# Kernel tuning notes

Hardware: AMD Instinct MI355X
Metric: run time of the kernel (lower is better)

Reference implementation:

```python
import jax, jax.numpy as jnp
import numpy as np

BN_EPS = 1e-5


def _tconv(X, w1, b1, w2, b2, w3, b3):
    # X: (B, T, N, C) -> conv over time with kernel (1, k), gated GLU-style
    Xp = X.transpose(0, 2, 1, 3)  # (B, N, T, C)
    def conv(w, b):
        return jax.lax.conv_general_dilated(
            Xp, w, (1, 1), 'VALID',
            dimension_numbers=('NHWC', 'HWIO', 'NHWC')) + b
    P = conv(w1, b1)
    Q = jax.nn.sigmoid(conv(w2, b2))
    R = conv(w3, b3)
    H = jax.nn.relu(P * Q + R)
    return H.transpose(0, 2, 1, 3)  # (B, T-k+1, N, Cout)


def _cheb(x, ei, W, b):
    # Batched ChebConv (sym norm, lambda_max=2 => L_hat = -D^-1/2 A D^-1/2)
    # x: (S, N, F), ei: (S, 2, E), W: (K, F, Fout)
    S, N, F = x.shape
    row, col = ei[:, 0], ei[:, 1]           # (S, E)
    ones = jnp.ones(ei.shape[-1], x.dtype)
    def norm_one(r, c):
        deg = jax.ops.segment_sum(ones, r, num_segments=N)
        dis = jnp.where(deg > 0, jax.lax.rsqrt(jnp.maximum(deg, 1.)), 0.)
        return -dis[r] * dis[c]
    w = jax.vmap(norm_one)(row, col)        # (S, E), constant wrt floats
    def prop(xs, r, c, ws):
        return jax.ops.segment_sum(ws[:, None] * xs[c], r, num_segments=N)
    propv = jax.vmap(prop)
    Tx = [x, propv(x, row, col, w)]
    for _ in range(W.shape[0] - 2):
        Tx.append(2. * propv(Tx[-1], row, col, w) - Tx[-2])
    return jnp.einsum('ksnf,kfo->sno', jnp.stack(Tx), W) + b


def _forward(X, tc1_w1, tc1_b1, tc1_w2, tc1_b2, tc1_w3, tc1_b3,
             cheb_w, cheb_b,
             tc2_w1, tc2_b1, tc2_w2, tc2_b2, tc2_w3, tc2_b3,
             bn_gamma, bn_beta, conv3_w, conv3_b, f1_w, f1_b, edge_index):
    T0 = _tconv(X, tc1_w1, tc1_b1, tc1_w2, tc1_b2, tc1_w3, tc1_b3)  # (B,38,N,H)
    B, Tt, N, H = T0.shape
    ei = edge_index[:, :Tt].reshape(B * Tt, 2, edge_index.shape[-1])
    G = _cheb(T0.reshape(B * Tt, N, H), ei, cheb_w, cheb_b)
    G = jax.nn.relu(G.reshape(B, Tt, N, H))
    T2 = _tconv(G, tc2_w1, tc2_b1, tc2_w2, tc2_b2, tc2_w3, tc2_b3)  # (B,36,N,Co)
    # BatchNorm2d over channel dim = num_nodes (training-mode batch stats)
    Tn = T2.transpose(0, 2, 1, 3)  # (B, N, T, C)
    mean = Tn.mean(axis=(0, 2, 3), keepdims=True)
    var = Tn.var(axis=(0, 2, 3), keepdims=True)
    Tn = (Tn - mean) * jax.lax.rsqrt(var + BN_EPS)
    Tn = Tn * bn_gamma[None, :, None, None] + bn_beta[None, :, None, None]
    Tb = Tn.transpose(0, 2, 1, 3)                 # (B, T, N, C)
    Tr = Tb.reshape(B, Tb.shape[1], -1)           # (B, T, N*C=3200)
    y = jax.lax.conv_general_dilated(
        Tr[:, None, :, :], conv3_w, (1, 1), 'VALID',
        dimension_numbers=('NCHW', 'OIHW', 'NCHW'))  # (B,128,T-2,1)
    y = y + conv3_b[None, :, None, None]
    y = y[:, :, :, 0]
    pooled = y.mean(axis=2)                        # AvgPool1d over full length
    return pooled @ f1_w + f1_b                    # (B, 3200)


def setup_inputs() -> dict:
    key = jax.random.key(0)
    ks = jax.random.split(key, 20)
    B, Tw, N, Cin, H, Co, E = 32, 40, 50, 2, 128, 64, 800
    KT, K = 3, 3
    s = 0.05
    d = {
        'X': jax.random.normal(ks[0], (B, Tw, N, Cin), jnp.float32),
        'edge_index': jax.random.randint(ks[1], (B, Tw, 2, E), 0, N),
        'tc1_w1': jax.random.normal(ks[2], (1, KT, Cin, H), jnp.float32) * s,
        'tc1_b1': jnp.zeros((H,), jnp.float32),
        'tc1_w2': jax.random.normal(ks[3], (1, KT, Cin, H), jnp.float32) * s,
        'tc1_b2': jnp.zeros((H,), jnp.float32),
        'tc1_w3': jax.random.normal(ks[4], (1, KT, Cin, H), jnp.float32) * s,
        'tc1_b3': jnp.zeros((H,), jnp.float32),
        'cheb_w': jax.random.normal(ks[5], (K, H, H), jnp.float32) * s,
        'cheb_b': jnp.zeros((H,), jnp.float32),
        'tc2_w1': jax.random.normal(ks[6], (1, KT, H, Co), jnp.float32) * s,
        'tc2_b1': jnp.zeros((Co,), jnp.float32),
        'tc2_w2': jax.random.normal(ks[7], (1, KT, H, Co), jnp.float32) * s,
        'tc2_b2': jnp.zeros((Co,), jnp.float32),
        'tc2_w3': jax.random.normal(ks[8], (1, KT, H, Co), jnp.float32) * s,
        'tc2_b3': jnp.zeros((Co,), jnp.float32),
        'bn_gamma': jnp.ones((N,), jnp.float32),
        'bn_beta': jnp.zeros((N,), jnp.float32),
        'conv3_w': jax.random.normal(ks[9], (128, 1, 3, N * Co), jnp.float32) * 0.01,
        'conv3_b': jnp.zeros((128,), jnp.float32),
        'f1_w': jax.random.normal(ks[10], (128, N * Co), jnp.float32) * s,
        'f1_b': jnp.zeros((N * Co,), jnp.float32),
    }
    return d


def reference(X, tc1_w1, tc1_b1, tc1_w2, tc1_b2, tc1_w3, tc1_b3,
              cheb_w, cheb_b,
              tc2_w1, tc2_b1, tc2_w2, tc2_b2, tc2_w3, tc2_b3,
              bn_gamma, bn_beta, conv3_w, conv3_b, f1_w, f1_b, edge_index):
    return _forward(X, tc1_w1, tc1_b1, tc1_w2, tc1_b2, tc1_w3, tc1_b3,
                    cheb_w, cheb_b,
                    tc2_w1, tc2_b1, tc2_w2, tc2_b2, tc2_w3, tc2_b3,
                    bn_gamma, bn_beta, conv3_w, conv3_b, f1_w, f1_b, edge_index)
```

## Files before the change

kernel.cpp:

```cpp
#include <hip/hip_runtime.h>
#include <hip/hip_bf16.h>

#define BB 32
#define TW 40
#define NN 50
#define HH 128
#define CO 64
#define EE 800
#define TT 38
#define TT2 36
#define TPOOL 34
#define NCO 3200
#define SS (BB*TT)
#define NPAD 64
#define RPAD (SS*NPAD)

#define PB_US ((size_t)RPAD * HH)
#define PB_BYTES (PB_US * 2)

typedef __attribute__((ext_vector_type(8))) short s16x8;
typedef __attribute__((ext_vector_type(16))) float f32x16;
typedef unsigned short us;

static __device__ __forceinline__ unsigned int f2bf_u(float x) {
    unsigned int u = __float_as_uint(x);
    return (u + 0x7fffu + ((u >> 16) & 1u)) >> 16;
}
static __device__ __forceinline__ float bfu2f(unsigned int h) {
    return __uint_as_float(h << 16);
}
static __device__ __forceinline__ size_t fragoff32(int m, int c) {
    return (size_t)(c >> 4) * 512 + ((c >> 3) & 1) * 256 + m * 8 + (c & 7);
}
#define MFMA(a, b, c) __builtin_amdgcn_mfma_f32_32x32x16_bf16((a), (b), (c), 0, 0, 0)

__global__ __launch_bounds__(256) void k_wprep(
    const float* __restrict__ cw,
    const float* __restrict__ tw1, const float* __restrict__ tw2, const float* __restrict__ tw3,
    us* __restrict__ VTh, us* __restrict__ VTl,
    us* __restrict__ WTh,
    float* __restrict__ pooled)
{
    int idx = blockIdx.x * 256 + threadIdx.x;
    float v; int col, k; bool wantlo;
    us *dh, *dl;
    if (idx < 128 * 384) {
        col = idx / 384; k = idx % 384;
        if (k < 128)      v = cw[k * 128 + col] - cw[32768 + k * 128 + col];
        else if (k < 256) v = cw[16384 + (k - 128) * 128 + col];
        else              v = 2.f * cw[32768 + (k - 256) * 128 + col];
        dh = VTh; dl = VTl; wantlo = true;
    } else if (idx < 128 * 384 + 192 * 384) {
        int i2 = idx - 128 * 384;
        col = i2 / 384; k = i2 % 384;
        int gg = col >> 6, o = col & 63;
        const float* src = (gg == 0) ? tw1 : (gg == 1) ? tw2 : tw3;
        v = src[k * 64 + o];
        dh = WTh; dl = 0; wantlo = false;
    } else {
        int z = idx - (128 * 384 + 192 * 384);
        if (z < 4096) pooled[z] = 0.f;
        return;
    }
    size_t off = ((size_t)((col >> 5) * 24 + (k >> 4)) * 64 + ((k >> 3) & 1) * 32 + (col & 31)) * 8
               + (k & 7);
    unsigned int h = f2bf_u(v);
    dh[off] = (us)h;
    if (wantlo) dl[off] = (us)f2bf_u(v - bfu2f(h));
}

#define TAS 136
#define TBS 72
#define LMS 53
__global__ __launch_bounds__(256) void k_cheb(
    const int* __restrict__ EI, const float* __restrict__ X,
    const float* __restrict__ w1, const float* __restrict__ b1,
    const float* __restrict__ w2, const float* __restrict__ b2,
    const float* __restrict__ w3, const float* __restrict__ b3,
    const us* __restrict__ VTh, const us* __restrict__ VTl,
    const float* __restrict__ bias,
    us* __restrict__ Gh)
{
    __shared__ __align__(16) char smem[61440];
    us* TbA = (us*)smem;
    us* TbB = (us*)(smem + 17408);
    us* Pa  = (us*)(smem + 35840);
    float* Lm = (float*)(smem + 35840);
    us* LA  = (us*)(smem + 53248);
    float* Xs = (float*)(smem + 53248);
    int* deg  = (int*)(smem + 53248 + 1216);
    float* dis = (float*)(smem + 53248 + 1216 + 224);

    int g = blockIdx.x;
    int tid = threadIdx.x;
    int b = g / TT, t = g % TT;
    const int* row = EI + (size_t)(b * TW + t) * 2 * EE;
    const int* col = row + EE;

    {
        s16x8 zz = {0, 0, 0, 0, 0, 0, 0, 0};
        for (int i = tid; i < 2240; i += 256) ((s16x8*)smem)[i] = zz;
    }
    for (int i = tid; i < 52 * LMS; i += 256) Lm[i] = 0.f;
    for (int i = tid; i < 300; i += 256) Xs[i] = X[(size_t)(b * TW + t) * 100 + i];
    if (tid < NN) deg[tid] = 0;
    __syncthreads();

    {
        int c = tid & 127, nh = tid >> 7;
        float wr1[6], wr2[6], wr3[6];
#pragma unroll
        for (int q = 0; q < 6; q++) {
            wr1[q] = w1[q * HH + c];
            wr2[q] = w2[q * HH + c];
            wr3[q] = w3[q * HH + c];
        }
        float bv1 = b1[c], bv2 = b2[c], bv3 = b3[c];
        for (int n = nh; n < NN; n += 2) {
            float P = bv1, Q = bv2, R = bv3;
#pragma unroll
            for (int q = 0; q < 6; q++) {
                float x = Xs[(q >> 1) * 100 + n * 2 + (q & 1)];
                P += x * wr1[q]; Q += x * wr2[q]; R += x * wr3[q];
            }
            float sg = 1.f / (1.f + expf(-Q));
            float v = P * sg + R;
            v = v > 0.f ? v : 0.f;
            us h = (us)f2bf_u(v);
            TbA[n * TAS + c] = h;
            TbB[c * TBS + n] = h;
        }
    }
    __syncthreads();
    for (int e = tid; e < EE; e += 256) atomicAdd(&deg[row[e]], 1);
    __syncthreads();
    if (tid < NN) dis[tid] = deg[tid] > 0 ? rsqrtf((float)deg[tid]) : 0.f;
    __syncthreads();
    for (int e = tid; e < EE; e += 256) {
        int r = row[e], cc = col[e];
        atomicAdd(&Lm[r * LMS + cc], -dis[r] * dis[cc]);
    }
    __syncthreads();
    for (int ent = tid; ent < 512; ent += 256) {
        int lanee = ent & 63;
        int ks = (ent >> 6) & 3;
        int mt = ent >> 8;
        int m = mt * 32 + (lanee & 31);
        int kb = ks * 16 + (lanee >> 5) * 8;
        s16x8 v;
#pragma unroll
        for (int j = 0; j < 8; j++) {
            int k = kb + j;
            float lv = (m < NN && k < NN) ? Lm[m * LMS + k] : 0.f;
            v[j] = (short)f2bf_u(lv);
        }
        *(s16x8*)(LA + ent * 8) = v;
    }
    __syncthreads();

    int lane = tid & 63;
    int w = tid >> 6;
    int rg = w >> 1, fh = w & 1;
    int nl = lane & 31;
    int khalf = lane >> 5;
    size_t laneoff = (size_t)lane * 8;

    const us* vh0 = VTh + (size_t)(fh * 2) * 12288 + laneoff;
    const us* vh1 = VTh + (size_t)(fh * 2 + 1) * 12288 + laneoff;
    const us* vl0 = VTl + (size_t)(fh * 2) * 12288 + laneoff;
    const us* vl1 = VTl + (size_t)(fh * 2 + 1) * 12288 + laneoff;

    int mrowA = rg * 32 + nl;
    int kbb = khalf * 8;

    f32x16 gacc0, gacc1, d0, d1;
#pragma unroll
    for (int r = 0; r < 16; r++) { gacc0[r] = 0.f; gacc1[r] = 0.f; d0[r] = 0.f; d1[r] = 0.f; }

#pragma unroll
    for (int ks = 0; ks < 4; ks++) {
        s16x8 afr = *(const s16x8*)(LA + ((rg * 4 + ks) * 64 + lane) * 8);
        int kb = ks * 16 + kbb;
        s16x8 bf0 = *(const s16x8*)(TbB + (fh * 64 + nl) * TBS + kb);
        s16x8 bf1 = *(const s16x8*)(TbB + (fh * 64 + 32 + nl) * TBS + kb);
        d0 = MFMA(afr, bf0, d0);
        d1 = MFMA(afr, bf1, d1);
    }
#pragma unroll
    for (int ks = 0; ks < 8; ks++) {
        s16x8 ah = *(const s16x8*)(TbA + mrowA * TAS + ks * 16 + kbb);
        s16x8 bh0 = *(const s16x8*)(vh0 + ks * 512);
        s16x8 bl0 = *(const s16x8*)(vl0 + ks * 512);
        s16x8 bh1 = *(const s16x8*)(vh1 + ks * 512);
        s16x8 bl1 = *(const s16x8*)(vl1 + ks * 512);
        gacc0 = MFMA(ah, bh0, gacc0); gacc0 = MFMA(ah, bl0, gacc0);
        gacc1 = MFMA(ah, bh1, gacc1); gacc1 = MFMA(ah, bl1, gacc1);
    }
    __syncthreads();
#pragma unroll
    for (int r = 0; r < 16; r++) {
        int mrow = (r & 3) + 8 * (r >> 2) + 4 * khalf;
        int node = rg * 32 + mrow;
        int f0 = fh * 64 + nl, f1 = f0 + 32;
        us h0 = (us)f2bf_u(d0[r]);
        us h1 = (us)f2bf_u(d1[r]);
        Pa[node * TAS + f0] = h0;
        Pa[node * TAS + f1] = h1;
        TbB[f0 * TBS + node] = h0;
        TbB[f1 * TBS + node] = h1;
    }
    __syncthreads();

#pragma unroll
    for (int r = 0; r < 16; r++) { d0[r] = 0.f; d1[r] = 0.f; }
#pragma unroll
    for (int ks = 0; ks < 4; ks++) {
        s16x8 afr = *(const s16x8*)(LA + ((rg * 4 + ks) * 64 + lane) * 8);
        int kb = ks * 16 + kbb;
        s16x8 bf0 = *(const s16x8*)(TbB + (fh * 64 + nl) * TBS + kb);
        s16x8 bf1 = *(const s16x8*)(TbB + (fh * 64 + 32 + nl) * TBS + kb);
        d0 = MFMA(afr, bf0, d0);
        d1 = MFMA(afr, bf1, d1);
    }
#pragma unroll
    for (int ks = 0; ks < 8; ks++) {
        s16x8 ah = *(const s16x8*)(Pa + mrowA * TAS + ks * 16 + kbb);
        s16x8 bh0 = *(const s16x8*)(vh0 + (8 + ks) * 512);
        s16x8 bh1 = *(const s16x8*)(vh1 + (8 + ks) * 512);
        gacc0 = MFMA(ah, bh0, gacc0);
        gacc1 = MFMA(ah, bh1, gacc1);
    }
    __syncthreads();
#pragma unroll
    for (int r = 0; r < 16; r++) {
        int mrow = (r & 3) + 8 * (r >> 2) + 4 * khalf;
        int node = rg * 32 + mrow;
        int f0 = fh * 64 + nl, f1 = f0 + 32;
        Pa[node * TAS + f0] = (us)f2bf_u(d0[r]);
        Pa[node * TAS + f1] = (us)f2bf_u(d1[r]);
    }
    __syncthreads();
#pragma unroll
    for (int ks = 0; ks < 8; ks++) {
        s16x8 ah = *(const s16x8*)(Pa + mrowA * TAS + ks * 16 + kbb);
        s16x8 bh0 = *(const s16x8*)(vh0 + (16 + ks) * 512);
        s16x8 bh1 = *(const s16x8*)(vh1 + (16 + ks) * 512);
        gacc0 = MFMA(ah, bh0, gacc0);
        gacc1 = MFMA(ah, bh1, gacc1);
    }

    int c0 = fh * 64 + nl, c1 = c0 + 32;
    float bv0 = bias[c0], bv1 = bias[c1];
    size_t gb = (size_t)g * 8192 + (size_t)rg * 4096;
#pragma unroll
    for (int r = 0; r < 16; r++) {
        int mrow = (r & 3) + 8 * (r >> 2) + 4 * khalf;
        float v0 = gacc0[r] + bv0; v0 = v0 > 0.f ? v0 : 0.f;
        float v1 = gacc1[r] + bv1; v1 = v1 > 0.f ? v1 : 0.f;
        Gh[gb + fragoff32(mrow, c0)] = (us)f2bf_u(v0);
        Gh[gb + fragoff32(mrow, c1)] = (us)f2bf_u(v1);
    }
}

__global__ __launch_bounds__(128) void k_tc2(
    const us* __restrict__ Gh,
    const us* __restrict__ WTh,
    const float* __restrict__ tb1, const float* __restrict__ tb2, const float* __restrict__ tb3,
    us* __restrict__ T2)
{
    int tid = threadIdx.x;
    int lane = tid & 63;
    int w = tid >> 6;
    int nl = lane & 31;
    size_t laneoff = (size_t)lane * 8;
    int i = blockIdx.x;
    int vb = (i & 7) * 288 + (i >> 3);
    int bt36 = vb >> 1, ntile = vb & 1;
    int b = bt36 / TT2, t = bt36 % TT2;

    const us* A[3];
#pragma unroll
    for (int k3 = 0; k3 < 3; k3++)
        A[k3] = Gh + (size_t)(b * TT + t + k3) * 8192 + (size_t)ntile * 4096 + laneoff;
    const us* Bh[3];
#pragma unroll
    for (int g3 = 0; g3 < 3; g3++)
        Bh[g3] = WTh + (size_t)(g3 * 2 + w) * 12288 + laneoff;

    f32x16 aP, aQ, aR;
#pragma unroll
    for (int r = 0; r < 16; r++) { aP[r] = 0.f; aQ[r] = 0.f; aR[r] = 0.f; }

#pragma unroll
    for (int k3 = 0; k3 < 3; k3++) {
#pragma unroll
        for (int ls = 0; ls < 8; ls++) {
            int offB = (k3 * 8 + ls) * 512;
            s16x8 a0 = *(const s16x8*)(A[k3] + ls * 512);
            s16x8 ph = *(const s16x8*)(Bh[0] + offB);
            s16x8 qh = *(const s16x8*)(Bh[1] + offB);
            s16x8 rh = *(const s16x8*)(Bh[2] + offB);
            aP = MFMA(a0, ph, aP);
            aQ = MFMA(a0, qh, aQ);
            aR = MFMA(a0, rh, aR);
        }
    }

    int o = w * 32 + nl;
    float bP = tb1[o], bQ = tb2[o], bR = tb3[o];
    int rbase = (lane >> 5) * 4;
#pragma unroll
    for (int r = 0; r < 16; r++) {
        int m = (r & 3) + 8 * (r >> 2) + rbase;
        int node = ntile * 32 + m;
        if (node < NN) {
            float P = aP[r] + bP, Q = aQ[r] + bQ, R = aR[r] + bR;
            float sg = 1.f / (1.f + expf(-Q));
            float v = P * sg + R;
            v = v > 0.f ? v : 0.f;
            T2[((size_t)bt36 * NN + node) * CO + o] = (us)f2bf_u(v);
        }
    }
}

__global__ __launch_bounds__(256) void k_bnpart(const us* __restrict__ T2, float* __restrict__ partial)
{
    int n = blockIdx.x >> 3, c = blockIdx.x & 7;
    int tid = threadIdx.x;
    float s = 0.f, ss = 0.f;
    for (int i = tid; i < 144 * 64; i += 256) {
        int bt = c * 144 + (i >> 6), o = i & 63;
        float v = bfu2f(T2[((size_t)bt * NN + n) * CO + o]);
        s += v; ss += v * v;
    }
    for (int off = 32; off > 0; off >>= 1) { s += __shfl_down(s, off, 64); ss += __shfl_down(ss, off, 64); }
    __shared__ float rs[4], rss[4];
    int lane = tid & 63, wv = tid >> 6;
    if (lane == 0) { rs[wv] = s; rss[wv] = ss; }
    __syncthreads();
    if (tid == 0) {
        partial[n * 8 + c] = rs[0] + rs[1] + rs[2] + rs[3];
        partial[400 + n * 8 + c] = rss[0] + rss[1] + rss[2] + rss[3];
    }
}

__global__ __launch_bounds__(64) void k_bnfin(const float* __restrict__ partial, float* __restrict__ stats)
{
    int n = threadIdx.x;
    if (n < NN) {
        float s = 0.f, ss = 0.f;
#pragma unroll
        for (int c = 0; c < 8; c++) { s += partial[n * 8 + c]; ss += partial[400 + n * 8 + c]; }
        const float inv = 1.f / (float)(BB * TT2 * CO);
        float m = s * inv;
        float var = ss * inv - m * m;
        stats[n] = m;
        stats[64 + n] = rsqrtf(var + 1e-5f);
    }
}

__global__ __launch_bounds__(256) void k_upool(
    const us* __restrict__ T2, const float* __restrict__ stats,
    const float* __restrict__ gamma, const float* __restrict__ beta,
    const float* __restrict__ W3, float* __restrict__ pooled)
{
    __shared__ __align__(16) float Ul[48 * 36 + 32];
    __shared__ float Ws[128 * 9];
    int blk = blockIdx.x;
    int jc = blk * 16;
    int n0 = jc >> 6;
    int tid = threadIdx.x;
    float mn = stats[n0], is = stats[64 + n0];
    float sc = is * gamma[n0];
    float off = (float)TPOOL * beta[n0] - (float)TPOOL * mn * sc;

    {
        int j = tid & 15, b0 = tid >> 4;
#pragma unroll
        for (int bp = 0; bp < 2; bp++) {
            int bb = b0 + 16 * bp;
            const us* p = T2 + (size_t)bb * TT2 * NCO + jc + j;
            float s0 = 0.f;
            for (int t = 0; t < TPOOL; t++) s0 += bfu2f(p[(size_t)t * NCO]);
            float s1 = s0 - bfu2f(p[0]) + bfu2f(p[(size_t)34 * NCO]);
            float s2 = s1 - bfu2f(p[(size_t)1 * NCO]) + bfu2f(p[(size_t)35 * NCO]);
            Ul[(0 * 16 + j) * 36 + bb] = s0 * sc + off;
            Ul[(1 * 16 + j) * 36 + bb] = s1 * sc + off;
            Ul[(2 * 16 + j) * 36 + bb] = s2 * sc + off;
        }
    }
    __syncthreads();

    int o = tid & 127, bq = tid >> 7;
    float acc[16];
#pragma unroll
    for (int i = 0; i < 16; i++) acc[i] = 0.f;

    for (int kjc = 0; kjc < 48; kjc += 8) {
        __syncthreads();
#pragma unroll
        for (int p4 = 0; p4 < 4; p4++) {
            int idx = p4 * 256 + tid;
            int oo = idx >> 3, q = idx & 7;
            int kj = kjc + q;
            Ws[oo * 9 + q] = W3[(size_t)oo * 9600 + (kj >> 4) * 3200 + jc + (kj & 15)];
        }
        __syncthreads();
#pragma unroll
        for (int q = 0; q < 8; q++) {
            float wv = Ws[o * 9 + q];
            const float* up = &Ul[(kjc + q) * 36 + bq * 16];
#pragma unroll
            for (int i4 = 0; i4 < 4; i4++) {
                float4 u = *(const float4*)(up + i4 * 4);
                acc[i4 * 4 + 0] += wv * u.x;
                acc[i4 * 4 + 1] += wv * u.y;
                acc[i4 * 4 + 2] += wv * u.z;
                acc[i4 * 4 + 3] += wv * u.w;
            }
        }
    }
#pragma unroll
    for (int i = 0; i < 16; i++)
        atomicAdd(&pooled[(size_t)(bq * 16 + i) * 128 + o], acc[i]);
}

__global__ __launch_bounds__(256) void k_final(
    const float* __restrict__ pooled, const float* __restrict__ b3c,
    const float* __restrict__ f1w, const float* __restrict__ f1b,
    float* __restrict__ out)
{
    __shared__ float pb[32 * 129];
    int tid = threadIdx.x;
    const float inv = 1.f / (float)TPOOL;
    for (int i = tid; i < 4096; i += 256) {
        int b = i >> 7, o = i & 127;
        pb[b * 129 + o] = pooled[b * 128 + o] * inv + b3c[o];
    }
    __syncthreads();
    int q = blockIdx.x * 8 + (tid & 7);
    int b = tid >> 3;
    float acc = f1b[q];
    const float* wq = f1w + q;
    const float* pbb = pb + b * 129;
#pragma unroll 4
    for (int o = 0; o < 128; o++) acc += pbb[o] * wq[(size_t)o * NCO];
    out[(size_t)b * NCO + q] = acc;
}

extern "C" void kernel_launch(void* const* d_in, const int* in_sizes, int n_in,
                              void* d_out, int out_size, void* d_ws, size_t ws_size,
                              hipStream_t stream)
{
    const float* X       = (const float*)d_in[0];
    const int*   EI      = (const int*)d_in[1];
    const float* tc1_w1  = (const float*)d_in[2];
    const float* tc1_b1  = (const float*)d_in[3];
    const float* tc1_w2  = (const float*)d_in[4];
    const float* tc1_b2  = (const float*)d_in[5];
    const float* tc1_w3  = (const float*)d_in[6];
    const float* tc1_b3  = (const float*)d_in[7];
    const float* cheb_w  = (const float*)d_in[8];
    const float* cheb_b  = (const float*)d_in[9];
    const float* tc2_w1  = (const float*)d_in[10];
    const float* tc2_b1  = (const float*)d_in[11];
    const float* tc2_w2  = (const float*)d_in[12];
    const float* tc2_b2  = (const float*)d_in[13];
    const float* tc2_w3  = (const float*)d_in[14];
    const float* tc2_b3  = (const float*)d_in[15];
    const float* bn_g    = (const float*)d_in[16];
    const float* bn_b    = (const float*)d_in[17];
    const float* conv3_w = (const float*)d_in[18];
    const float* conv3_b = (const float*)d_in[19];
    const float* f1_w    = (const float*)d_in[20];
    const float* f1_b    = (const float*)d_in[21];

    char* base = (char*)d_ws;
    us*    Gh     = (us*)base;
    us*    T2     = (us*)(base + PB_BYTES);
    float* pooled = (float*)(base + PB_BYTES + 7372800);
    float* stats  = (float*)(base + PB_BYTES + 7389184);
    float* partial= (float*)(base + PB_BYTES + 7389696);
    us*    VTh    = (us*)(base + PB_BYTES + 7392896);
    us*    VTl    = VTh + 49152;
    us*    WTh    = VTl + 49152;

    k_wprep<<<496, 256, 0, stream>>>(cheb_w, tc2_w1, tc2_w2, tc2_w3, VTh, VTl, WTh, pooled);
    k_cheb<<<SS, 256, 0, stream>>>(EI, X, tc1_w1, tc1_b1, tc1_w2, tc1_b2, tc1_w3, tc1_b3,
                                   VTh, VTl, cheb_b, Gh);
    k_tc2<<<2304, 128, 0, stream>>>(Gh, WTh, tc2_b1, tc2_b2, tc2_b3, T2);
    k_bnpart<<<NN * 8, 256, 0, stream>>>(T2, partial);
    k_bnfin<<<1, 64, 0, stream>>>(partial, stats);
    k_upool<<<200, 256, 0, stream>>>(T2, stats, bn_g, bn_b, conv3_w, pooled);
    k_final<<<NCO / 8, 256, 0, stream>>>(pooled, conv3_b, f1_w, f1_b, (float*)d_out);
}
```

Before: 221.9 us.

## Fuse batchnorm statistics into pooling kernel and flatten final linear kernel

```diff
diff --git a/kernel.cpp b/kernel.cpp
--- a/kernel.cpp
+++ b/kernel.cpp
@@ -323,71 +323,58 @@
     }
 }
 
-__global__ __launch_bounds__(256) void k_bnpart(const us* __restrict__ T2, float* __restrict__ partial)
-{
-    int n = blockIdx.x >> 3, c = blockIdx.x & 7;
-    int tid = threadIdx.x;
-    float s = 0.f, ss = 0.f;
-    for (int i = tid; i < 144 * 64; i += 256) {
-        int bt = c * 144 + (i >> 6), o = i & 63;
-        float v = bfu2f(T2[((size_t)bt * NN + n) * CO + o]);
-        s += v; ss += v * v;
-    }
-    for (int off = 32; off > 0; off >>= 1) { s += __shfl_down(s, off, 64); ss += __shfl_down(ss, off, 64); }
-    __shared__ float rs[4], rss[4];
-    int lane = tid & 63, wv = tid >> 6;
-    if (lane == 0) { rs[wv] = s; rss[wv] = ss; }
-    __syncthreads();
-    if (tid == 0) {
-        partial[n * 8 + c] = rs[0] + rs[1] + rs[2] + rs[3];
-        partial[400 + n * 8 + c] = rss[0] + rss[1] + rss[2] + rss[3];
-    }
-}
-
-__global__ __launch_bounds__(64) void k_bnfin(const float* __restrict__ partial, float* __restrict__ stats)
-{
-    int n = threadIdx.x;
-    if (n < NN) {
-        float s = 0.f, ss = 0.f;
-#pragma unroll
-        for (int c = 0; c < 8; c++) { s += partial[n * 8 + c]; ss += partial[400 + n * 8 + c]; }
-        const float inv = 1.f / (float)(BB * TT2 * CO);
-        float m = s * inv;
-        float var = ss * inv - m * m;
-        stats[n] = m;
-        stats[64 + n] = rsqrtf(var + 1e-5f);
-    }
-}
-
+#define UPST 129
 __global__ __launch_bounds__(256) void k_upool(
-    const us* __restrict__ T2, const float* __restrict__ stats,
+    const us* __restrict__ T2,
     const float* __restrict__ gamma, const float* __restrict__ beta,
     const float* __restrict__ W3, float* __restrict__ pooled)
 {
-    __shared__ __align__(16) float Ul[48 * 36 + 32];
-    __shared__ float Ws[128 * 9];
+    __shared__ float Ws[96 * UPST];
+    __shared__ __align__(16) float Ul[96 * 36];
+    __shared__ float red[512];
     int blk = blockIdx.x;
-    int jc = blk * 16;
-    int n0 = jc >> 6;
+    int n = blk >> 1, jh = blk & 1;
     int tid = threadIdx.x;
-    float mn = stats[n0], is = stats[64 + n0];
-    float sc = is * gamma[n0];
-    float off = (float)TPOOL * beta[n0] - (float)TPOOL * mn * sc;
-
-    {
-        int j = tid & 15, b0 = tid >> 4;
-#pragma unroll
-        for (int bp = 0; bp < 2; bp++) {
-            int bb = b0 + 16 * bp;
-            const us* p = T2 + (size_t)bb * TT2 * NCO + jc + j;
-            float s0 = 0.f;
-            for (int t = 0; t < TPOOL; t++) s0 += bfu2f(p[(size_t)t * NCO]);
-            float s1 = s0 - bfu2f(p[0]) + bfu2f(p[(size_t)34 * NCO]);
-            float s2 = s1 - bfu2f(p[(size_t)1 * NCO]) + bfu2f(p[(size_t)35 * NCO]);
-            Ul[(0 * 16 + j) * 36 + bb] = s0 * sc + off;
-            Ul[(1 * 16 + j) * 36 + bb] = s1 * sc + off;
-            Ul[(2 * 16 + j) * 36 + bb] = s2 * sc + off;
-        }
+
+    for (int i = tid; i < 12288; i += 256) {
+        int ok = i >> 5, j = i & 31;
+        int o = ok / 3, k = ok - 3 * o;
+        Ws[(k * 32 + j) * UPST + o] = W3[(size_t)o * 9600 + k * 3200 + n * 64 + jh * 32 + j];
+    }
+
+    float s = 0.f, ss = 0.f;
+    for (int i = tid; i < 9216; i += 256) {
+        int bt = i >> 3, j8 = i & 7;
+        s16x8 v = *(const s16x8*)(T2 + (size_t)bt * 3200 + n * 64 + j8 * 8);
+#pragma unroll
+        for (int j = 0; j < 8; j++) {
+            float f = bfu2f((us)v[j]);
+            s += f; ss += f * f;
+        }
+    }
+    red[tid] = s; red[256 + tid] = ss;
+    __syncthreads();
+    for (int off = 128; off > 0; off >>= 1) {
+        if (tid < off) { red[tid] += red[tid + off]; red[256 + tid] += red[256 + tid + off]; }
+        __syncthreads();
+    }
+    const float inv = 1.f / (float)(BB * TT2 * CO);
+    float mn = red[0] * inv;
+    float var = red[256] * inv - mn * mn;
+    float sc = rsqrtf(var + 1e-5f) * gamma[n];
+    float offv = (float)TPOOL * beta[n] - (float)TPOOL * mn * sc;
+    __syncthreads();
+
+    for (int p = tid; p < 1024; p += 256) {
+        int j = p & 31, b = p >> 5;
+        const us* q = T2 + (size_t)b * 115200 + n * 64 + jh * 32 + j;
+        float s0 = 0.f;
+        for (int t = 0; t < TPOOL; t++) s0 += bfu2f(q[(size_t)t * 3200]);
+        float s1 = s0 - bfu2f(q[0]) + bfu2f(q[(size_t)34 * 3200]);
+        float s2 = s1 - bfu2f(q[(size_t)1 * 3200]) + bfu2f(q[(size_t)35 * 3200]);
+        Ul[(0 * 32 + j) * 36 + b] = s0 * sc + offv;
+        Ul[(1 * 32 + j) * 36 + b] = s1 * sc + offv;
+        Ul[(2 * 32 + j) * 36 + b] = s2 * sc + offv;
     }
     __syncthreads();
 
@@ -395,29 +382,16 @@
     float acc[16];
 #pragma unroll
     for (int i = 0; i < 16; i++) acc[i] = 0.f;
-
-    for (int kjc = 0; kjc < 48; kjc += 8) {
-        __syncthreads();
-#pragma unroll
-        for (int p4 = 0; p4 < 4; p4++) {
-            int idx = p4 * 256 + tid;
-            int oo = idx >> 3, q = idx & 7;
-            int kj = kjc + q;
-            Ws[oo * 9 + q] = W3[(size_t)oo * 9600 + (kj >> 4) * 3200 + jc + (kj & 15)];
-        }
-        __syncthreads();
-#pragma unroll
-        for (int q = 0; q < 8; q++) {
-            float wv = Ws[o * 9 + q];
-            const float* up = &Ul[(kjc + q) * 36 + bq * 16];
-#pragma unroll
-            for (int i4 = 0; i4 < 4; i4++) {
-                float4 u = *(const float4*)(up + i4 * 4);
-                acc[i4 * 4 + 0] += wv * u.x;
-                acc[i4 * 4 + 1] += wv * u.y;
-                acc[i4 * 4 + 2] += wv * u.z;
-                acc[i4 * 4 + 3] += wv * u.w;
-            }
+    for (int kj = 0; kj < 96; kj++) {
+        float wv = Ws[kj * UPST + o];
+        const float* up = &Ul[kj * 36 + bq * 16];
+#pragma unroll
+        for (int i4 = 0; i4 < 4; i4++) {
+            float4 u = *(const float4*)(up + i4 * 4);
+            acc[i4 * 4 + 0] += wv * u.x;
+            acc[i4 * 4 + 1] += wv * u.y;
+            acc[i4 * 4 + 2] += wv * u.z;
+            acc[i4 * 4 + 3] += wv * u.w;
         }
     }
 #pragma unroll
@@ -430,22 +404,16 @@
     const float* __restrict__ f1w, const float* __restrict__ f1b,
     float* __restrict__ out)
 {
-    __shared__ float pb[32 * 129];
-    int tid = threadIdx.x;
+    int idx = blockIdx.x * 256 + threadIdx.x;
+    if (idx >= BB * NCO) return;
+    int q = idx % NCO;
+    int b = idx / NCO;
     const float inv = 1.f / (float)TPOOL;
-    for (int i = tid; i < 4096; i += 256) {
-        int b = i >> 7, o = i & 127;
-        pb[b * 129 + o] = pooled[b * 128 + o] * inv + b3c[o];
-    }
-    __syncthreads();
-    int q = blockIdx.x * 8 + (tid & 7);
-    int b = tid >> 3;
     float acc = f1b[q];
-    const float* wq = f1w + q;
-    const float* pbb = pb + b * 129;
+    const float* pp = pooled + b * 128;
 #pragma unroll 4
-    for (int o = 0; o < 128; o++) acc += pbb[o] * wq[(size_t)o * NCO];
-    out[(size_t)b * NCO + q] = acc;
+    for (int o = 0; o < 128; o++) acc += (pp[o] * inv + b3c[o]) * f1w[(size_t)o * NCO + q];
+    out[idx] = acc;
 }
 
 extern "C" void kernel_launch(void* const* d_in, const int* in_sizes, int n_in,
@@ -479,9 +447,7 @@
     us*    Gh     = (us*)base;
     us*    T2     = (us*)(base + PB_BYTES);
     float* pooled = (float*)(base + PB_BYTES + 7372800);
-    float* stats  = (float*)(base + PB_BYTES + 7389184);
-    float* partial= (float*)(base + PB_BYTES + 7389696);
-    us*    VTh    = (us*)(base + PB_BYTES + 7392896);
+    us*    VTh    = (us*)(base + PB_BYTES + 7389184);
     us*    VTl    = VTh + 49152;
     us*    WTh    = VTl + 49152;
 
@@ -489,8 +455,6 @@
     k_cheb<<<SS, 256, 0, stream>>>(EI, X, tc1_w1, tc1_b1, tc1_w2, tc1_b2, tc1_w3, tc1_b3,
                                    VTh, VTl, cheb_b, Gh);
     k_tc2<<<2304, 128, 0, stream>>>(Gh, WTh, tc2_b1, tc2_b2, tc2_b3, T2);
-    k_bnpart<<<NN * 8, 256, 0, stream>>>(T2, partial);
-    k_bnfin<<<1, 64, 0, stream>>>(partial, stats);
-    k_upool<<<200, 256, 0, stream>>>(T2, stats, bn_g, bn_b, conv3_w, pooled);
-    k_final<<<NCO / 8, 256, 0, stream>>>(pooled, conv3_b, f1_w, f1_b, (float*)d_out);
-}
+    k_upool<<<100, 256, 0, stream>>>(T2, bn_g, bn_b, conv3_w, pooled);
+    k_final<<<(BB * NCO + 255) / 256, 256, 0, stream>>>(pooled, conv3_b, f1_w, f1_b, (float*)d_out);
+}
```

Measured after the change: 222.1 us. No clear change (+0.1%).
